# Kernel optimization log

Hardware: AMD Instinct MI355X
Metric: run time of the kernel (lower is better)

The kernel has to match this reference:

```python
import jax, jax.numpy as jnp
import numpy as np

N_FREQ = 48  # tcnn Frequency encoding n_frequencies


def _freq_encode(x):
    # x: [N,3] in [0,1]; tcnn Frequency: sin/cos of x * 2^f * pi, f=0..F-1
    freqs = (2.0 ** jnp.arange(N_FREQ, dtype=jnp.float32)) * jnp.pi  # [F]
    ang = x[:, :, None] * freqs  # [N,3,F]
    enc = jnp.stack([jnp.sin(ang), jnp.cos(ang)], axis=-1)  # [N,3,F,2]
    return enc.reshape(x.shape[0], -1)  # [N, 3*F*2]


def _bilinear_sample(plane, coords):
    # plane: [R,R,F] (H,W,feat); coords: [N,2] in [-1,1], coords[:,0]->width(x), coords[:,1]->height(y)
    # matches torch grid_sample(align_corners=True, bilinear) for in-range coords
    R = plane.shape[0]
    gx = (coords[:, 0] + 1.0) * 0.5 * (R - 1)
    gy = (coords[:, 1] + 1.0) * 0.5 * (R - 1)
    x0f = jnp.clip(jnp.floor(gx), 0.0, R - 1)
    y0f = jnp.clip(jnp.floor(gy), 0.0, R - 1)
    x0 = x0f.astype(jnp.int32)
    y0 = y0f.astype(jnp.int32)
    x1 = jnp.minimum(x0 + 1, R - 1)
    y1 = jnp.minimum(y0 + 1, R - 1)
    wx = (gx - x0f)[:, None]
    wy = (gy - y0f)[:, None]
    v00 = plane[y0, x0]
    v01 = plane[y0, x1]
    v10 = plane[y1, x0]
    v11 = plane[y1, x1]
    return (v00 * (1 - wx) * (1 - wy) + v01 * wx * (1 - wy)
            + v10 * (1 - wx) * wy + v11 * wx * wy)  # [N,F]


def setup_inputs() -> dict:
    key = jax.random.key(0)
    ks = jax.random.split(key, 8)
    N = 524288
    res, fdim = 32, 16
    enc_dim = 3 * N_FREQ * 2  # 288
    d_in = enc_dim + fdim     # 304
    h = 64
    positions = jax.random.uniform(ks[0], (N, 3), dtype=jnp.float32)
    aabb = jnp.array([0.0, 0.0, 0.0, 1.0, 1.0, 1.0], dtype=jnp.float32)
    triplane = jax.random.normal(ks[1], (3, res, res, fdim), dtype=jnp.float32) * 0.001
    W0 = jax.random.normal(ks[2], (d_in, h), dtype=jnp.float32) / np.sqrt(d_in)
    W1 = jax.random.normal(ks[3], (h, h), dtype=jnp.float32) / np.sqrt(h)
    W2 = jax.random.normal(ks[4], (h, h), dtype=jnp.float32) / np.sqrt(h)
    W3 = jax.random.normal(ks[5], (h, 4), dtype=jnp.float32) / np.sqrt(h)
    return {"positions": positions, "aabb": aabb, "triplane": triplane,
            "W0": W0, "W1": W1, "W2": W2, "W3": W3}


def reference(positions, aabb, triplane, W0, W1, W2, W3):
    aabb_min, aabb_max = aabb[:3], aabb[3:]
    xn = (positions - aabb_min) / (aabb_max - aabb_min)          # normalized [0,1]
    sc = 2.0 * xn - 1.0                                          # scaled_coords in [-1,1]
    selector = jnp.all((xn > 0.0) & (xn < 1.0), axis=-1)
    # plane coordinate pairs as in the torch code
    coords = jnp.stack([
        jnp.stack([sc[:, 0], sc[:, 1]], axis=1),  # xy
        jnp.stack([sc[:, 0], sc[:, 2]], axis=1),  # xz
        jnp.stack([sc[:, 1], sc[:, 2]], axis=1),  # zy
    ], axis=0)  # [3,N,2]
    feats = jax.vmap(_bilinear_sample)(triplane, coords).sum(0)  # [N,fdim]
    h = jnp.concatenate([_freq_encode(xn), feats], axis=1)       # [N,304]
    h = jnp.sin(h @ W0)
    h = jnp.sin(h @ W1)
    h = jnp.sin(h @ W2)
    out = h @ W3                                                 # [N,4]
    rgb = jax.nn.sigmoid(out[:, :3])
    density = jnp.exp(out[:, 3:4] - 1.0) * selector[:, None]     # trunc_exp(x-1)
    return rgb, density
```

## Files before the change

kernel.cpp:

```cpp
#include <hip/hip_runtime.h>
#include <stdint.h>

typedef _Float16 half8 __attribute__((ext_vector_type(8)));
typedef float f32x4 __attribute__((ext_vector_type(4)));

#define TPW 8
#define WPB 8
#define NT  512

static __device__ __forceinline__ void wave_fence() {
    __builtin_amdgcn_wave_barrier();
    asm volatile("" ::: "memory");
}

__device__ __forceinline__ float bf2f(uint16_t u) {
    return __uint_as_float(((uint32_t)u) << 16);
}
__device__ __forceinline__ uint16_t f2bf(float f) {
    uint32_t u = __float_as_uint(f);
    u = (u + 0x7FFFu + ((u >> 16) & 1u)) >> 16;
    return (uint16_t)u;
}

template<bool BF>
__device__ __forceinline__ float lde(const void* p, uint32_t i) {
    if constexpr (BF) return bf2f(((const uint16_t*)p)[i]);
    else              return ((const float*)p)[i];
}
template<bool BF>
__device__ __forceinline__ void st1(void* p, uint32_t i, float v) {
    if constexpr (BF) ((uint16_t*)p)[i] = f2bf(v);
    else              ((float*)p)[i] = v;
}
template<bool BF>
__device__ __forceinline__ void ld8(const void* p, uint32_t i, float* o) {
    if constexpr (BF) {
        const uint4 c = *(const uint4*)((const uint16_t*)p + i);
        const uint32_t* pu = (const uint32_t*)&c;
#pragma unroll
        for (int j = 0; j < 4; ++j) {
            o[2 * j]     = __uint_as_float(pu[j] << 16);
            o[2 * j + 1] = __uint_as_float(pu[j] & 0xFFFF0000u);
        }
    } else {
        const float4 a = *(const float4*)((const float*)p + i);
        const float4 b = *(const float4*)((const float*)p + i + 4);
        o[0] = a.x; o[1] = a.y; o[2] = a.z; o[3] = a.w;
        o[4] = b.x; o[5] = b.y; o[6] = b.z; o[7] = b.w;
    }
}

template<bool BF>
__device__ __forceinline__ void run_all(
    const void* __restrict__ posg, const void* __restrict__ aabbg,
    const void* __restrict__ tpg,
    const void* __restrict__ w0g, const void* __restrict__ w1g,
    const void* __restrict__ w2g, const void* __restrict__ w3g,
    void* __restrict__ outp, int npts,
    _Float16* w0t, _Float16* w1t, _Float16* w2t, _Float16* w3t, _Float16* hbuf)
{
    const int tid = threadIdx.x;
    const float I2PI = 0.15915494309189535f;

    for (int e = tid; e < 64 * 24; e += NT) { int n = e / 24, k = 304 + e % 24; w0t[n * 328 + k] = (_Float16)0.0f; }
    for (int e = tid; e < 16 * 72; e += NT) w3t[e] = (_Float16)0.0f;
    for (int e = tid; e < 304 * 64; e += NT) { int k = e >> 6, n = e & 63; w0t[n * 328 + k] = (_Float16)(lde<BF>(w0g, e) * I2PI); }
    for (int e = tid; e < 64 * 64;  e += NT) { int k = e >> 6, n = e & 63; w1t[n * 72 + k] = (_Float16)(lde<BF>(w1g, e) * I2PI);
                                               w2t[n * 72 + k] = (_Float16)(lde<BF>(w2g, e) * I2PI); }
    __syncthreads();
    for (int e = tid; e < 64 * 4;   e += NT) { int k = e >> 2, n = e & 3;  w3t[n * 72 + k] = (_Float16)lde<BF>(w3g, e); }
    __syncthreads();

    const int w = tid >> 6, lane = tid & 63;
    const int m = lane & 15, q = lane >> 4;
    _Float16* hb = hbuf + w * (16 * 72);

    const float mn0 = lde<BF>(aabbg, 0), mn1 = lde<BF>(aabbg, 1), mn2 = lde<BF>(aabbg, 2);
    const float mx0 = lde<BF>(aabbg, 3), mx1 = lde<BF>(aabbg, 4), mx2 = lde<BF>(aabbg, 5);

    const double IH = 0x1.45f306dc9c883p-2;
    const double IL = -0x1.6b01ec5417056p-56;
    const float PIF  = 3.14159274101257324f;
    const f32x4 z4 = {0.f, 0.f, 0.f, 0.f};

    for (int it = 0; it < TPW; ++it) {
        const int tile = (blockIdx.x * WPB + w) * TPW + it;
        const int base = tile * 16;
        const int pt = base + m;

        const float p0 = lde<BF>(posg, 3 * pt + 0);
        const float p1 = lde<BF>(posg, 3 * pt + 1);
        const float p2 = lde<BF>(posg, 3 * pt + 2);
        float xn[3];
        xn[0] = (p0 - mn0) / (mx0 - mn0);
        xn[1] = (p1 - mn1) / (mx1 - mn1);
        xn[2] = (p2 - mn2) / (mx2 - mn2);

        const bool sel = xn[0] > 0.f && xn[0] < 1.f && xn[1] > 0.f && xn[1] < 1.f
                      && xn[2] > 0.f && xn[2] < 1.f;
        const unsigned long long bm = __ballot(sel);

        double wh[3], wl[3];
#pragma unroll
        for (int d = 0; d < 3; ++d) {
            const float mf = xn[d] * PIF;
            const double md = (double)mf;
            const double hi = md * IH;
            const double r  = __builtin_fma(md, IH, -hi);
            wh[d] = hi;
            wl[d] = __builtin_fma(md, IL, r);
        }

        float fe[8];
#pragma unroll
        for (int j = 0; j < 8; ++j) fe[j] = 0.f;
        if (q < 2) {
            const int fo = q * 8;
            float g[3];
#pragma unroll
            for (int d = 0; d < 3; ++d) g[d] = xn[d] * 31.f;
            float v[8];
#pragma unroll
            for (int p = 0; p < 3; ++p) {
                const float gx = (p == 2) ? g[1] : g[0];
                const float gy = (p == 0) ? g[1] : g[2];
                const float x0f = fminf(fmaxf(floorf(gx), 0.f), 31.f);
                const float y0f = fminf(fmaxf(floorf(gy), 0.f), 31.f);
                const int x0 = (int)x0f, y0 = (int)y0f;
                int x1 = x0 + 1; if (x1 > 31) x1 = 31;
                int y1 = y0 + 1; if (y1 > 31) y1 = 31;
                const float wx = gx - x0f, wy = gy - y0f;
                const float w00 = (1.f - wx) * (1.f - wy);
                const float w01 = wx * (1.f - wy);
                const float w10 = (1.f - wx) * wy;
                const float w11 = wx * wy;
                const uint32_t pb = p * 16384 + fo;
                ld8<BF>(tpg, pb + y0 * 512 + x0 * 16, v);
#pragma unroll
                for (int j = 0; j < 8; ++j) fe[j] += v[j] * w00;
                ld8<BF>(tpg, pb + y0 * 512 + x1 * 16, v);
#pragma unroll
                for (int j = 0; j < 8; ++j) fe[j] += v[j] * w01;
                ld8<BF>(tpg, pb + y1 * 512 + x0 * 16, v);
#pragma unroll
                for (int j = 0; j < 8; ++j) fe[j] += v[j] * w10;
                ld8<BF>(tpg, pb + y1 * 512 + x1 * 16, v);
#pragma unroll
                for (int j = 0; j < 8; ++j) fe[j] += v[j] * w11;
            }
        }

        f32x4 acc[4] = {z4, z4, z4, z4};
#pragma unroll
        for (int d = 0; d < 3; ++d) {
#pragma unroll
            for (int cc = 0; cc < 3; ++cc) {
                const int e0 = 16 * cc + 4 * q - 1;
                const double zp = __builtin_bit_cast(double, (uint64_t)(1023 + e0) << 52);
                const double z  = wh[d] * zp;
                const double zl = wl[d] * zp;
                const double fr = z - __builtin_floor(z);
                const float t = (float)(fr + zl);
                float s = __builtin_amdgcn_sinf(t);
                float c = __builtin_amdgcn_cosf(t);
                half8 a;
                a[0] = (_Float16)s; a[1] = (_Float16)c;
#pragma unroll
                for (int jj = 1; jj < 4; ++jj) {
                    const float t2 = s + s;
                    const float sn = t2 * c;
                    c = __builtin_fmaf(-t2, s, 1.0f);
                    s = sn;
                    a[2 * jj]     = (_Float16)s;
                    a[2 * jj + 1] = (_Float16)c;
                }
                const int ch = 3 * d + cc;
#pragma unroll
                for (int t4 = 0; t4 < 4; ++t4) {
                    const half8 b = *(const half8*)&w0t[(t4 * 16 + m) * 328 + ch * 32 + q * 8];
                    acc[t4] = __builtin_amdgcn_mfma_f32_16x16x32_f16(a, b, acc[t4], 0, 0, 0);
                }
            }
        }
        {
            half8 a;
#pragma unroll
            for (int j = 0; j < 8; ++j) a[j] = (q < 2) ? (_Float16)fe[j] : (_Float16)0.f;
#pragma unroll
            for (int t4 = 0; t4 < 4; ++t4) {
                const half8 b = *(const half8*)&w0t[(t4 * 16 + m) * 328 + 288 + q * 8];
                acc[t4] = __builtin_amdgcn_mfma_f32_16x16x32_f16(a, b, acc[t4], 0, 0, 0);
            }
        }

#pragma unroll
        for (int t4 = 0; t4 < 4; ++t4)
#pragma unroll
            for (int rg = 0; rg < 4; ++rg)
                hb[(4 * q + rg) * 72 + t4 * 16 + m] =
                    (_Float16)__builtin_amdgcn_sinf(acc[t4][rg]);
        wave_fence();

        f32x4 acc2[4] = {z4, z4, z4, z4};
#pragma unroll
        for (int c = 0; c < 2; ++c) {
            const half8 a = *(const half8*)&hb[m * 72 + c * 32 + q * 8];
#pragma unroll
            for (int t4 = 0; t4 < 4; ++t4) {
                const half8 b = *(const half8*)&w1t[(t4 * 16 + m) * 72 + c * 32 + q * 8];
                acc2[t4] = __builtin_amdgcn_mfma_f32_16x16x32_f16(a, b, acc2[t4], 0, 0, 0);
            }
        }
        wave_fence();
#pragma unroll
        for (int t4 = 0; t4 < 4; ++t4)
#pragma unroll
            for (int rg = 0; rg < 4; ++rg)
                hb[(4 * q + rg) * 72 + t4 * 16 + m] =
                    (_Float16)__builtin_amdgcn_sinf(acc2[t4][rg]);
        wave_fence();

        f32x4 accx[4] = {z4, z4, z4, z4};
#pragma unroll
        for (int c = 0; c < 2; ++c) {
            const half8 a = *(const half8*)&hb[m * 72 + c * 32 + q * 8];
#pragma unroll
            for (int t4 = 0; t4 < 4; ++t4) {
                const half8 b = *(const half8*)&w2t[(t4 * 16 + m) * 72 + c * 32 + q * 8];
                accx[t4] = __builtin_amdgcn_mfma_f32_16x16x32_f16(a, b, accx[t4], 0, 0, 0);
            }
        }
        wave_fence();
#pragma unroll
        for (int t4 = 0; t4 < 4; ++t4)
#pragma unroll
            for (int rg = 0; rg < 4; ++rg)
                hb[(4 * q + rg) * 72 + t4 * 16 + m] =
                    (_Float16)__builtin_amdgcn_sinf(accx[t4][rg]);
        wave_fence();

        f32x4 acc3 = z4;
#pragma unroll
        for (int c = 0; c < 2; ++c) {
            const half8 a = *(const half8*)&hb[m * 72 + c * 32 + q * 8];
            const half8 b = *(const half8*)&w3t[m * 72 + c * 32 + q * 8];
            acc3 = __builtin_amdgcn_mfma_f32_16x16x32_f16(a, b, acc3, 0, 0, 0);
        }
        wave_fence();

        if (m < 3) {
#pragma unroll
            for (int rg = 0; rg < 4; ++rg) {
                const float s = 1.f / (1.f + __expf(-acc3[rg]));
                st1<BF>(outp, (uint32_t)(base + 4 * q + rg) * 3u + m, s);
            }
        } else if (m == 3) {
#pragma unroll
            for (int rg = 0; rg < 4; ++rg) {
                float dens = __expf(acc3[rg] - 1.f);
                if (!((bm >> (4 * q + rg)) & 1ull)) dens = 0.f;
                st1<BF>(outp, 3u * (uint32_t)npts + (uint32_t)(base + 4 * q + rg), dens);
            }
        }
    }
}

__global__ __launch_bounds__(NT, 4)
void tri_mlp(const void* __restrict__ posg, const void* __restrict__ aabbg,
             const void* __restrict__ tpg,
             const void* __restrict__ w0g, const void* __restrict__ w1g,
             const void* __restrict__ w2g, const void* __restrict__ w3g,
             void* __restrict__ outp, int npts)
{
    __shared__ alignas(16) _Float16 w0t[64 * 328];
    __shared__ alignas(16) _Float16 w1t[64 * 72];
    __shared__ alignas(16) _Float16 w2t[64 * 72];
    __shared__ alignas(16) _Float16 w3t[16 * 72];
    __shared__ alignas(16) _Float16 hbuf[WPB * 16 * 72];

    const bool bf = (((const uint32_t*)aabbg)[2] != 0u);
    if (bf) run_all<true >(posg, aabbg, tpg, w0g, w1g, w2g, w3g, outp, npts, w0t, w1t, w2t, w3t, hbuf);
    else    run_all<false>(posg, aabbg, tpg, w0g, w1g, w2g, w3g, outp, npts, w0t, w1t, w2t, w3t, hbuf);
}

extern "C" void kernel_launch(void* const* d_in, const int* in_sizes, int n_in,
                              void* d_out, int out_size, void* d_ws, size_t ws_size,
                              hipStream_t stream) {
    const int npts = in_sizes[0] / 3;
    const int blocks = npts / (16 * WPB * TPW);
    tri_mlp<<<blocks, NT, 0, stream>>>(d_in[0], d_in[1], d_in[2], d_in[3],
                                       d_in[4], d_in[5], d_in[6], d_out, npts);
}
```

Before: 149.6 us.

## Swizzle hidden-state LDS layout, prefetch positions, pack f16 converts, vectorize density stores

```diff
diff --git a/kernel.cpp b/kernel.cpp
--- a/kernel.cpp
+++ b/kernel.cpp
@@ -1,12 +1,17 @@
 #include <hip/hip_runtime.h>
 #include <stdint.h>
 
-typedef _Float16 half8 __attribute__((ext_vector_type(8)));
+typedef _Float16 half8  __attribute__((ext_vector_type(8)));
+typedef _Float16 half2v __attribute__((ext_vector_type(2)));
 typedef float f32x4 __attribute__((ext_vector_type(4)));
 
 #define TPW 8
 #define WPB 8
 #define NT  512
+
+__device__ __forceinline__ half2v pkrtz(float a, float b) {
+    return __builtin_bit_cast(half2v, __builtin_amdgcn_cvt_pkrtz(a, b));
+}
 
 static __device__ __forceinline__ void wave_fence() {
     __builtin_amdgcn_wave_barrier();
@@ -48,6 +53,10 @@
         o[0] = a.x; o[1] = a.y; o[2] = a.z; o[3] = a.w;
         o[4] = b.x; o[5] = b.y; o[6] = b.z; o[7] = b.w;
     }
+}
+
+__device__ __forceinline__ int hswz(int p, int g) {
+    return p * 72 + ((g + 2 * (p >> 2)) & 7) * 8;
 }
 
 template<bool BF>
@@ -83,14 +92,27 @@
     const float PIF  = 3.14159274101257324f;
     const f32x4 z4 = {0.f, 0.f, 0.f, 0.f};
 
+    const int tile0 = (blockIdx.x * WPB + w) * TPW;
+
+    float cp0, cp1, cp2;
+    {
+        const int pt = tile0 * 16 + m;
+        cp0 = lde<BF>(posg, 3 * pt + 0);
+        cp1 = lde<BF>(posg, 3 * pt + 1);
+        cp2 = lde<BF>(posg, 3 * pt + 2);
+    }
+
     for (int it = 0; it < TPW; ++it) {
-        const int tile = (blockIdx.x * WPB + w) * TPW + it;
-        const int base = tile * 16;
-        const int pt = base + m;
-
-        const float p0 = lde<BF>(posg, 3 * pt + 0);
-        const float p1 = lde<BF>(posg, 3 * pt + 1);
-        const float p2 = lde<BF>(posg, 3 * pt + 2);
+        const int base = (tile0 + it) * 16;
+        const float p0 = cp0, p1 = cp1, p2 = cp2;
+        {
+            const int nit = (it + 1 < TPW) ? it + 1 : it;
+            const int pt2 = (tile0 + nit) * 16 + m;
+            cp0 = lde<BF>(posg, 3 * pt2 + 0);
+            cp1 = lde<BF>(posg, 3 * pt2 + 1);
+            cp2 = lde<BF>(posg, 3 * pt2 + 2);
+        }
+
         float xn[3];
         xn[0] = (p0 - mn0) / (mx0 - mn0);
         xn[1] = (p1 - mn1) / (mx1 - mn1);
@@ -163,48 +185,55 @@
                 const float t = (float)(fr + zl);
                 float s = __builtin_amdgcn_sinf(t);
                 float c = __builtin_amdgcn_cosf(t);
-                half8 a;
-                a[0] = (_Float16)s; a[1] = (_Float16)c;
+                union { half8 h8; half2v h2[4]; } au;
+                au.h2[0] = pkrtz(s, c);
 #pragma unroll
                 for (int jj = 1; jj < 4; ++jj) {
                     const float t2 = s + s;
                     const float sn = t2 * c;
                     c = __builtin_fmaf(-t2, s, 1.0f);
                     s = sn;
-                    a[2 * jj]     = (_Float16)s;
-                    a[2 * jj + 1] = (_Float16)c;
+                    au.h2[jj] = pkrtz(s, c);
                 }
                 const int ch = 3 * d + cc;
 #pragma unroll
                 for (int t4 = 0; t4 < 4; ++t4) {
                     const half8 b = *(const half8*)&w0t[(t4 * 16 + m) * 328 + ch * 32 + q * 8];
-                    acc[t4] = __builtin_amdgcn_mfma_f32_16x16x32_f16(a, b, acc[t4], 0, 0, 0);
+                    acc[t4] = __builtin_amdgcn_mfma_f32_16x16x32_f16(au.h8, b, acc[t4], 0, 0, 0);
                 }
             }
         }
         {
-            half8 a;
-#pragma unroll
-            for (int j = 0; j < 8; ++j) a[j] = (q < 2) ? (_Float16)fe[j] : (_Float16)0.f;
+            union { half8 h8; half2v h2[4]; } au;
+            if (q < 2) {
+#pragma unroll
+                for (int i = 0; i < 4; ++i)
+                    au.h2[i] = pkrtz(fe[2 * i], fe[2 * i + 1]);
+            } else {
+#pragma unroll
+                for (int j = 0; j < 8; ++j) au.h8[j] = (_Float16)0.f;
+            }
 #pragma unroll
             for (int t4 = 0; t4 < 4; ++t4) {
                 const half8 b = *(const half8*)&w0t[(t4 * 16 + m) * 328 + 288 + q * 8];
-                acc[t4] = __builtin_amdgcn_mfma_f32_16x16x32_f16(a, b, acc[t4], 0, 0, 0);
-            }
-        }
-
-#pragma unroll
-        for (int t4 = 0; t4 < 4; ++t4)
+                acc[t4] = __builtin_amdgcn_mfma_f32_16x16x32_f16(au.h8, b, acc[t4], 0, 0, 0);
+            }
+        }
+
+#pragma unroll
+        for (int t4 = 0; t4 < 4; ++t4) {
+            const int gw = 2 * t4 + (m >> 3);
 #pragma unroll
             for (int rg = 0; rg < 4; ++rg)
-                hb[(4 * q + rg) * 72 + t4 * 16 + m] =
+                hb[hswz(4 * q + rg, gw) + (m & 7)] =
                     (_Float16)__builtin_amdgcn_sinf(acc[t4][rg]);
+        }
         wave_fence();
 
         f32x4 acc2[4] = {z4, z4, z4, z4};
 #pragma unroll
         for (int c = 0; c < 2; ++c) {
-            const half8 a = *(const half8*)&hb[m * 72 + c * 32 + q * 8];
+            const half8 a = *(const half8*)&hb[hswz(m, 4 * c + q)];
 #pragma unroll
             for (int t4 = 0; t4 < 4; ++t4) {
                 const half8 b = *(const half8*)&w1t[(t4 * 16 + m) * 72 + c * 32 + q * 8];
@@ -213,17 +242,19 @@
         }
         wave_fence();
 #pragma unroll
-        for (int t4 = 0; t4 < 4; ++t4)
+        for (int t4 = 0; t4 < 4; ++t4) {
+            const int gw = 2 * t4 + (m >> 3);
 #pragma unroll
             for (int rg = 0; rg < 4; ++rg)
-                hb[(4 * q + rg) * 72 + t4 * 16 + m] =
+                hb[hswz(4 * q + rg, gw) + (m & 7)] =
                     (_Float16)__builtin_amdgcn_sinf(acc2[t4][rg]);
+        }
         wave_fence();
 
         f32x4 accx[4] = {z4, z4, z4, z4};
 #pragma unroll
         for (int c = 0; c < 2; ++c) {
-            const half8 a = *(const half8*)&hb[m * 72 + c * 32 + q * 8];
+            const half8 a = *(const half8*)&hb[hswz(m, 4 * c + q)];
 #pragma unroll
             for (int t4 = 0; t4 < 4; ++t4) {
                 const half8 b = *(const half8*)&w2t[(t4 * 16 + m) * 72 + c * 32 + q * 8];
@@ -232,17 +263,19 @@
         }
         wave_fence();
 #pragma unroll
-        for (int t4 = 0; t4 < 4; ++t4)
+        for (int t4 = 0; t4 < 4; ++t4) {
+            const int gw = 2 * t4 + (m >> 3);
 #pragma unroll
             for (int rg = 0; rg < 4; ++rg)
-                hb[(4 * q + rg) * 72 + t4 * 16 + m] =
+                hb[hswz(4 * q + rg, gw) + (m & 7)] =
                     (_Float16)__builtin_amdgcn_sinf(accx[t4][rg]);
+        }
         wave_fence();
 
         f32x4 acc3 = z4;
 #pragma unroll
         for (int c = 0; c < 2; ++c) {
-            const half8 a = *(const half8*)&hb[m * 72 + c * 32 + q * 8];
+            const half8 a = *(const half8*)&hb[hswz(m, 4 * c + q)];
             const half8 b = *(const half8*)&w3t[m * 72 + c * 32 + q * 8];
             acc3 = __builtin_amdgcn_mfma_f32_16x16x32_f16(a, b, acc3, 0, 0, 0);
         }
@@ -255,17 +288,28 @@
                 st1<BF>(outp, (uint32_t)(base + 4 * q + rg) * 3u + m, s);
             }
         } else if (m == 3) {
+            float dv[4];
 #pragma unroll
             for (int rg = 0; rg < 4; ++rg) {
                 float dens = __expf(acc3[rg] - 1.f);
                 if (!((bm >> (4 * q + rg)) & 1ull)) dens = 0.f;
-                st1<BF>(outp, 3u * (uint32_t)npts + (uint32_t)(base + 4 * q + rg), dens);
+                dv[rg] = dens;
+            }
+            const uint32_t di = 3u * (uint32_t)npts + (uint32_t)(base + 4 * q);
+            if constexpr (BF) {
+                ushort4 pk;
+                pk.x = f2bf(dv[0]); pk.y = f2bf(dv[1]);
+                pk.z = f2bf(dv[2]); pk.w = f2bf(dv[3]);
+                *(ushort4*)((uint16_t*)outp + di) = pk;
+            } else {
+                float4 pk = {dv[0], dv[1], dv[2], dv[3]};
+                *(float4*)((float*)outp + di) = pk;
             }
         }
     }
 }
 
-__global__ __launch_bounds__(NT, 4)
+__global__ __launch_bounds__(NT) __attribute__((amdgpu_waves_per_eu(4, 4)))
 void tri_mlp(const void* __restrict__ posg, const void* __restrict__ aabbg,
              const void* __restrict__ tpg,
              const void* __restrict__ w0g, const void* __restrict__ w1g,
```

Result: faster. 146.4 us (-2.1%).
